# Kernel optimization log

Hardware: AMD Instinct MI355X
Metric: run time of the kernel (lower is better)

## Reference

```python
import jax, jax.numpy as jnp
import numpy as np

INPUT_DIM = 2048
NUM_EXPERTS = 64
TOP_K = 2


def setup_inputs() -> dict:
    key = jax.random.key(0)
    kx, kw, kb = jax.random.split(key, 3)
    x = jax.random.normal(kx, (4, 4096, INPUT_DIM), dtype=jnp.float32)
    # nn.Linear default init: U(-1/sqrt(fan_in), 1/sqrt(fan_in))
    bound = 1.0 / np.sqrt(INPUT_DIM)
    W = jax.random.uniform(kw, (INPUT_DIM, NUM_EXPERTS), dtype=jnp.float32, minval=-bound, maxval=bound)
    b = jax.random.uniform(kb, (NUM_EXPERTS,), dtype=jnp.float32, minval=-bound, maxval=bound)
    return {"x": x, "W": W, "b": b}


def reference(x, W, b):
    # router_logits = Linear(x); p = softmax(logits, -1); topk over experts
    logits = jnp.einsum("bsd,de->bse", x, W) + b          # [B, S, E]
    p = jax.nn.softmax(logits, axis=-1)                     # [B, S, E]
    gate_vals, expert_idx = jax.lax.top_k(p, TOP_K)         # [B, S, k] each
    return expert_idx, gate_vals
```

## Files before the change

### kernel.cpp

```cpp
#include <hip/hip_runtime.h>
#include <hip/hip_bf16.h>
#include <math.h>


#define DIM 2048
#define NE 64

typedef __attribute__((ext_vector_type(8))) short short8;
typedef __attribute__((ext_vector_type(4))) float floatx4;

__device__ __forceinline__ short bf16bits(float v) {
  __hip_bfloat16 h = __float2bfloat16(v);
  return *(short*)&h;
}
__device__ __forceinline__ float bf16tof(short s) {
  union { unsigned int u; float f; } c;
  c.u = ((unsigned int)(unsigned short)s) << 16;
  return c.f;
}

__global__ void wprep_kernel(const float* __restrict__ W, short8* __restrict__ wf) {
  const int s = blockIdx.x >> 2, n = blockIdx.x & 3, l = threadIdx.x;
  const int d0 = s * 32 + (l >> 4) * 8;
  const int e = n * 16 + (l & 15);
  short8 vh, vl;
#pragma unroll
  for (int j = 0; j < 8; ++j) {
    float v = W[(size_t)(d0 + j) * NE + e];
    short h = bf16bits(v);
    vh[j] = h;
    vl[j] = bf16bits(v - bf16tof(h));
  }
  wf[(size_t)((s * 4 + n) * 2 + 0) * 64 + l] = vh;
  wf[(size_t)((s * 4 + n) * 2 + 1) * 64 + l] = vl;
}

__device__ __forceinline__ void async_copy16(const float* g, void* lds) {
  __builtin_amdgcn_global_load_lds(
      (const __attribute__((address_space(1))) unsigned int*)g,
      (__attribute__((address_space(3))) unsigned int*)lds, 16, 0, 0);
}

__global__ __launch_bounds__(256, 3) void router_main(
    const float* __restrict__ x, const short8* __restrict__ wf,
    const float* __restrict__ b, float* __restrict__ out, int ntok) {
  __shared__ alignas(16) char smem[33280];
  const int tid = threadIdx.x;
  const int lane = tid & 63;
  const int kq = tid >> 6;
  const int g = lane & 15, r4 = lane >> 4;
  const int tok0 = blockIdx.x * 32;

  char* mybuf = smem + kq * 8192;
  const float* xb = x + (size_t)tok0 * DIM + kq * 512;

  auto issue = [&](int c, char* dst) {
    const float* gb = xb + c * 32;
#pragma unroll
    for (int p = 0; p < 4; ++p) {
      const int rr = p * 8 + (lane >> 3);
      const float* gp = gb + (size_t)rr * DIM + ((((lane & 7) - rr) & 7) << 2);
      async_copy16(gp, dst + p * 1024);
    }
  };

  floatx4 acc[2][4];
#pragma unroll
  for (int mt = 0; mt < 2; ++mt)
#pragma unroll
    for (int n = 0; n < 4; ++n) acc[mt][n] = (floatx4){0.f, 0.f, 0.f, 0.f};

  issue(0, mybuf);

  for (int c = 0; c < 16; ++c) {
    const int sg = kq * 16 + c;
    const short8* wp = wf + (size_t)sg * 8 * 64;
    short8 Wh[4], Wl[4];
#pragma unroll
    for (int n = 0; n < 4; ++n) {
      Wh[n] = wp[(n * 2 + 0) * 64 + lane];
      Wl[n] = wp[(n * 2 + 1) * 64 + lane];
    }
    if (c < 15) issue(c + 1, mybuf + ((c + 1) & 1) * 4096);
    asm volatile("s_waitcnt vmcnt(4)" ::: "memory");

    const float* bb = (const float*)(mybuf + (c & 1) * 4096);
#pragma unroll
    for (int mt = 0; mt < 2; ++mt) {
      const int row = mt * 16 + g;
      const int ga0 = r4 * 2;
      floatx4 a0 = *(const floatx4*)(bb + row * 32 + (((ga0 + 0 + row) & 7) << 2));
      floatx4 a1 = *(const floatx4*)(bb + row * 32 + (((ga0 + 1 + row) & 7) << 2));
      short8 Ah, Al;
#pragma unroll
      for (int j = 0; j < 4; ++j) {
        short h = bf16bits(a0[j]);
        Ah[j] = h; Al[j] = bf16bits(a0[j] - bf16tof(h));
      }
#pragma unroll
      for (int j = 0; j < 4; ++j) {
        short h = bf16bits(a1[j]);
        Ah[4 + j] = h; Al[4 + j] = bf16bits(a1[j] - bf16tof(h));
      }
#pragma unroll
      for (int n = 0; n < 4; ++n) {
        acc[mt][n] = __builtin_amdgcn_mfma_f32_16x16x32_bf16(Ah, Wh[n], acc[mt][n], 0, 0, 0);
        acc[mt][n] = __builtin_amdgcn_mfma_f32_16x16x32_bf16(Ah, Wl[n], acc[mt][n], 0, 0, 0);
        acc[mt][n] = __builtin_amdgcn_mfma_f32_16x16x32_bf16(Al, Wh[n], acc[mt][n], 0, 0, 0);
      }
    }
  }

  __syncthreads();
  float* red = (float*)smem;
#pragma unroll
  for (int mt = 0; mt < 2; ++mt)
#pragma unroll
    for (int n = 0; n < 4; ++n)
#pragma unroll
      for (int r = 0; r < 4; ++r) {
        const int tokl = mt * 16 + r4 * 4 + r;
        const int e = n * 16 + g;
        red[(kq * 32 + tokl) * 65 + e] = acc[mt][n][r];
      }
  __syncthreads();

  {
    const int tl = lane & 7, er = lane >> 3;
    const int t = kq * 8 + tl;
    float lv[8];
    float v1 = -INFINITY, v2 = -INFINITY;
    int i1 = 0, i2 = 0;
#pragma unroll
    for (int i = 0; i < 8; ++i) {
      const int e = er * 8 + i;
      float v = red[t * 65 + e] + red[(32 + t) * 65 + e] +
                red[(64 + t) * 65 + e] + red[(96 + t) * 65 + e] + b[e];
      lv[i] = v;
      if (v > v1) { v2 = v1; i2 = i1; v1 = v; i1 = e; }
      else if (v > v2) { v2 = v; i2 = e; }
    }
#pragma unroll
    for (int off = 8; off < 64; off <<= 1) {
      float ov1 = __shfl_xor(v1, off, 64); int oi1 = __shfl_xor(i1, off, 64);
      float ov2 = __shfl_xor(v2, off, 64); int oi2 = __shfl_xor(i2, off, 64);
      bool aw = (v1 > ov1) || (v1 == ov1 && i1 < oi1);
      float nv1 = aw ? v1 : ov1; int ni1 = aw ? i1 : oi1;
      float c2v = aw ? ov1 : v1; int c2i = aw ? oi1 : i1;
      float w2v = aw ? v2 : ov2; int w2i = aw ? i2 : oi2;
      bool sw = (w2v > c2v) || (w2v == c2v && w2i < c2i);
      v2 = sw ? w2v : c2v; i2 = sw ? w2i : c2i;
      v1 = nv1; i1 = ni1;
    }
    float s = 0.f;
#pragma unroll
    for (int i = 0; i < 8; ++i) s += __expf(lv[i] - v1);
#pragma unroll
    for (int off = 8; off < 64; off <<= 1) s += __shfl_xor(s, off, 64);
    if (er == 0) {
      const int tok = tok0 + t;
      out[tok * 2 + 0] = (float)i1;
      out[tok * 2 + 1] = (float)i2;
      out[ntok * 2 + tok * 2 + 0] = 1.0f / s;
      out[ntok * 2 + tok * 2 + 1] = __expf(v2 - v1) / s;
    }
  }
}

extern "C" void kernel_launch(void* const* d_in, const int* in_sizes, int n_in,
                              void* d_out, int out_size, void* d_ws, size_t ws_size,
                              hipStream_t stream) {
  const float* x = (const float*)d_in[0];
  const float* W = (const float*)d_in[1];
  const float* b = (const float*)d_in[2];
  float* out = (float*)d_out;
  const int ntok = in_sizes[0] / DIM;
  short8* wf = (short8*)d_ws;

  wprep_kernel<<<256, 64, 0, stream>>>(W, wf);
  router_main<<<ntok / 32, 256, 0, stream>>>(x, wf, b, out, ntok);
}
```

Measured before the change: 199.2 us.

## Split K across four blocks and move softmax/top-k into a separate kernel

The GEMM is split along the input dimension into four blocks per 32-token group, which quadruples the grid. Each block loads its 32x512 slice of x into LDS in one shot instead of running a double-buffered pipeline, and writes partial logits to workspace. A new second kernel sums the four partials, adds the bias and does softmax and top-2. The aim is more parallelism and memory-level concurrency for the bandwidth-bound x read. The cost is an extra launch, a global round trip for the partials, and lower occupancy from the larger LDS buffer.

```diff
diff --git a/kernel.cpp b/kernel.cpp
--- a/kernel.cpp
+++ b/kernel.cpp
@@ -5,6 +5,7 @@
 
 #define DIM 2048
 #define NE 64
+#define RSTRIDE 2064
 
 typedef __attribute__((ext_vector_type(8))) short short8;
 typedef __attribute__((ext_vector_type(4))) float floatx4;
@@ -41,28 +42,26 @@
       (__attribute__((address_space(3))) unsigned int*)lds, 16, 0, 0);
 }
 
-__global__ __launch_bounds__(256, 3) void router_main(
+__global__ __launch_bounds__(256, 2) void router_gemm(
     const float* __restrict__ x, const short8* __restrict__ wf,
-    const float* __restrict__ b, float* __restrict__ out, int ntok) {
-  __shared__ alignas(16) char smem[33280];
-  const int tid = threadIdx.x;
-  const int lane = tid & 63;
-  const int kq = tid >> 6;
+    float* __restrict__ part) {
+  __shared__ alignas(16) char smem[32 * RSTRIDE];
+  const int tid = threadIdx.x, lane = tid & 63, kq = tid >> 6;
   const int g = lane & 15, r4 = lane >> 4;
-  const int tok0 = blockIdx.x * 32;
+  const int gblk = blockIdx.x >> 2, s = blockIdx.x & 3;
+  const int tok0 = gblk * 32;
 
-  char* mybuf = smem + kq * 8192;
-  const float* xb = x + (size_t)tok0 * DIM + kq * 512;
-
-  auto issue = [&](int c, char* dst) {
-    const float* gb = xb + c * 32;
+  {
+    const float* xb = x + (size_t)tok0 * DIM + s * 512;
 #pragma unroll
-    for (int p = 0; p < 4; ++p) {
-      const int rr = p * 8 + (lane >> 3);
-      const float* gp = gb + (size_t)rr * DIM + ((((lane & 7) - rr) & 7) << 2);
-      async_copy16(gp, dst + p * 1024);
+    for (int r = 0; r < 8; ++r) {
+      const int row = kq * 8 + r;
+      const float* rp = xb + (size_t)row * DIM;
+      char* dst = smem + row * RSTRIDE;
+      async_copy16(rp + lane * 4, dst);
+      async_copy16(rp + 256 + lane * 4, dst + 1024);
     }
-  };
+  }
 
   floatx4 acc[2][4];
 #pragma unroll
@@ -70,10 +69,11 @@
 #pragma unroll
     for (int n = 0; n < 4; ++n) acc[mt][n] = (floatx4){0.f, 0.f, 0.f, 0.f};
 
-  issue(0, mybuf);
+  __syncthreads();
 
-  for (int c = 0; c < 16; ++c) {
-    const int sg = kq * 16 + c;
+#pragma unroll
+  for (int step = 0; step < 4; ++step) {
+    const int sg = s * 16 + kq * 4 + step;
     const short8* wp = wf + (size_t)sg * 8 * 64;
     short8 Wh[4], Wl[4];
 #pragma unroll
@@ -81,16 +81,13 @@
       Wh[n] = wp[(n * 2 + 0) * 64 + lane];
       Wl[n] = wp[(n * 2 + 1) * 64 + lane];
     }
-    if (c < 15) issue(c + 1, mybuf + ((c + 1) & 1) * 4096);
-    asm volatile("s_waitcnt vmcnt(4)" ::: "memory");
-
-    const float* bb = (const float*)(mybuf + (c & 1) * 4096);
+    const int colb = kq * 512 + step * 128 + r4 * 32;
 #pragma unroll
     for (int mt = 0; mt < 2; ++mt) {
       const int row = mt * 16 + g;
-      const int ga0 = r4 * 2;
-      floatx4 a0 = *(const floatx4*)(bb + row * 32 + (((ga0 + 0 + row) & 7) << 2));
-      floatx4 a1 = *(const floatx4*)(bb + row * 32 + (((ga0 + 1 + row) & 7) << 2));
+      const float* ap = (const float*)(smem + row * RSTRIDE + colb);
+      floatx4 a0 = *(const floatx4*)ap;
+      floatx4 a1 = *(const floatx4*)(ap + 4);
       short8 Ah, Al;
 #pragma unroll
       for (int j = 0; j < 4; ++j) {
@@ -125,45 +122,63 @@
       }
   __syncthreads();
 
-  {
-    const int tl = lane & 7, er = lane >> 3;
-    const int t = kq * 8 + tl;
-    float lv[8];
-    float v1 = -INFINITY, v2 = -INFINITY;
-    int i1 = 0, i2 = 0;
+  float* pblk = part + (size_t)blockIdx.x * 2048;
 #pragma unroll
-    for (int i = 0; i < 8; ++i) {
-      const int e = er * 8 + i;
-      float v = red[t * 65 + e] + red[(32 + t) * 65 + e] +
-                red[(64 + t) * 65 + e] + red[(96 + t) * 65 + e] + b[e];
-      lv[i] = v;
-      if (v > v1) { v2 = v1; i2 = i1; v1 = v; i1 = e; }
-      else if (v > v2) { v2 = v; i2 = e; }
-    }
+  for (int i = tid; i < 512; i += 256) {
+    const int f = i * 4, tok = f >> 6, e0 = f & 63;
+    floatx4 v;
 #pragma unroll
-    for (int off = 8; off < 64; off <<= 1) {
-      float ov1 = __shfl_xor(v1, off, 64); int oi1 = __shfl_xor(i1, off, 64);
-      float ov2 = __shfl_xor(v2, off, 64); int oi2 = __shfl_xor(i2, off, 64);
-      bool aw = (v1 > ov1) || (v1 == ov1 && i1 < oi1);
-      float nv1 = aw ? v1 : ov1; int ni1 = aw ? i1 : oi1;
-      float c2v = aw ? ov1 : v1; int c2i = aw ? oi1 : i1;
-      float w2v = aw ? v2 : ov2; int w2i = aw ? i2 : oi2;
-      bool sw = (w2v > c2v) || (w2v == c2v && w2i < c2i);
-      v2 = sw ? w2v : c2v; i2 = sw ? w2i : c2i;
-      v1 = nv1; i1 = ni1;
-    }
-    float s = 0.f;
+    for (int j = 0; j < 4; ++j)
+      v[j] = red[(tok) * 65 + e0 + j] + red[(32 + tok) * 65 + e0 + j] +
+             red[(64 + tok) * 65 + e0 + j] + red[(96 + tok) * 65 + e0 + j];
+    *(floatx4*)(pblk + f) = v;
+  }
+}
+
+__global__ __launch_bounds__(256) void router_topk(
+    const float* __restrict__ part, const float* __restrict__ b,
+    float* __restrict__ out, int ntok) {
+  const int tid = threadIdx.x;
+  const int T = blockIdx.x * 16 + (tid >> 4);
+  const int eq = tid & 15, e0 = eq * 4;
+  const float* pb = part + ((size_t)(T >> 5) * 4) * 2048 + (T & 31) * 64 + e0;
+  floatx4 a = (floatx4){0.f, 0.f, 0.f, 0.f};
 #pragma unroll
-    for (int i = 0; i < 8; ++i) s += __expf(lv[i] - v1);
+  for (int s = 0; s < 4; ++s) a += *(const floatx4*)(pb + (size_t)s * 2048);
+  floatx4 bb = *(const floatx4*)(b + e0);
+  float lv[4];
+  float v1 = -INFINITY, v2 = -INFINITY;
+  int i1 = 0, i2 = 0;
 #pragma unroll
-    for (int off = 8; off < 64; off <<= 1) s += __shfl_xor(s, off, 64);
-    if (er == 0) {
-      const int tok = tok0 + t;
-      out[tok * 2 + 0] = (float)i1;
-      out[tok * 2 + 1] = (float)i2;
-      out[ntok * 2 + tok * 2 + 0] = 1.0f / s;
-      out[ntok * 2 + tok * 2 + 1] = __expf(v2 - v1) / s;
-    }
+  for (int j = 0; j < 4; ++j) {
+    float v = a[j] + bb[j];
+    lv[j] = v;
+    const int e = e0 + j;
+    if (v > v1) { v2 = v1; i2 = i1; v1 = v; i1 = e; }
+    else if (v > v2) { v2 = v; i2 = e; }
+  }
+#pragma unroll
+  for (int off = 1; off < 16; off <<= 1) {
+    float ov1 = __shfl_xor(v1, off, 64); int oi1 = __shfl_xor(i1, off, 64);
+    float ov2 = __shfl_xor(v2, off, 64); int oi2 = __shfl_xor(i2, off, 64);
+    bool aw = (v1 > ov1) || (v1 == ov1 && i1 < oi1);
+    float nv1 = aw ? v1 : ov1; int ni1 = aw ? i1 : oi1;
+    float c2v = aw ? ov1 : v1; int c2i = aw ? oi1 : i1;
+    float w2v = aw ? v2 : ov2; int w2i = aw ? i2 : oi2;
+    bool sw = (w2v > c2v) || (w2v == c2v && w2i < c2i);
+    v2 = sw ? w2v : c2v; i2 = sw ? w2i : c2i;
+    v1 = nv1; i1 = ni1;
+  }
+  float se = 0.f;
+#pragma unroll
+  for (int j = 0; j < 4; ++j) se += __expf(lv[j] - v1);
+#pragma unroll
+  for (int off = 1; off < 16; off <<= 1) se += __shfl_xor(se, off, 64);
+  if (eq == 0) {
+    out[T * 2 + 0] = (float)i1;
+    out[T * 2 + 1] = (float)i2;
+    out[ntok * 2 + T * 2 + 0] = 1.0f / se;
+    out[ntok * 2 + T * 2 + 1] = __expf(v2 - v1) / se;
   }
 }
 
@@ -176,7 +191,9 @@
   float* out = (float*)d_out;
   const int ntok = in_sizes[0] / DIM;
   short8* wf = (short8*)d_ws;
+  float* part = (float*)((char*)d_ws + 512 * 1024);
 
   wprep_kernel<<<256, 64, 0, stream>>>(W, wf);
-  router_main<<<ntok / 32, 256, 0, stream>>>(x, wf, b, out, ntok);
+  router_gemm<<<(ntok / 32) * 4, 256, 0, stream>>>(x, wf, part);
+  router_topk<<<ntok / 16, 256, 0, stream>>>(part, b, out, ntok);
 }
```

New measurement: 206.8 us. 3.9% more time.
